# Kernel tuning notes

Hardware: AMD Instinct MI355X
Metric: run time of the kernel (lower is better)

The kernel has to match this reference:

```python
import jax, jax.numpy as jnp
import numpy as np

LN_EPS = 1e-5


def setup_inputs() -> dict:
    key = jax.random.key(0)
    ks = jax.random.split(key, 6)
    B, I, H = 16384, 512, 512
    x = jax.random.normal(ks[0], (B, I), dtype=jnp.float32)
    h_prev = jax.random.normal(ks[1], (B, H), dtype=jnp.float32)
    c_prev = jax.random.normal(ks[2], (B, H), dtype=jnp.float32)
    # packed gate weights in i|f|g|o order (equivalent to 8 separate matmuls)
    W_i = jax.random.normal(ks[3], (I, 4 * H), dtype=jnp.float32) * (1.0 / np.sqrt(I))
    W_h = jax.random.normal(ks[4], (H, 4 * H), dtype=jnp.float32) * (1.0 / np.sqrt(H))
    # biases: b_i=0, b_f=1, b_g=0, b_o=0 as in the torch module
    b = jnp.concatenate([jnp.zeros(H), jnp.ones(H), jnp.zeros(H), jnp.zeros(H)]).astype(jnp.float32)
    ln_weight = jnp.ones((H,), dtype=jnp.float32)
    ln_bias = jnp.zeros((H,), dtype=jnp.float32)
    return {"x": x, "h_prev": h_prev, "c_prev": c_prev, "W_i": W_i, "W_h": W_h,
            "b": b, "ln_weight": ln_weight, "ln_bias": ln_bias}


def layer_norm(h, w, bias):
    mu = jnp.mean(h, axis=-1, keepdims=True)
    var = jnp.var(h, axis=-1, keepdims=True)
    return (h - mu) * jax.lax.rsqrt(var + LN_EPS) * w + bias


def reference(x, h_prev, c_prev, W_i, W_h, b, ln_weight, ln_bias):
    H = h_prev.shape[-1]
    # two fused GEMMs covering all 4 gates: [B, 4H]
    gates = x @ W_i + h_prev @ W_h + b
    i, f, g, o = jnp.split(gates, 4, axis=-1)
    i = jax.nn.sigmoid(i)
    f = jax.nn.sigmoid(f)
    g = jnp.tanh(g)
    o = jax.nn.sigmoid(o)
    c = f * c_prev + i * g
    h = o * jnp.tanh(c)
    h = layer_norm(h, ln_weight, ln_bias)
    return (h, c)
```

## Files before the change

### kernel.cpp

```cpp
#include <hip/hip_runtime.h>
#include <cstdint>
#include <cstddef>

typedef unsigned short ushort_t;
typedef __attribute__((ext_vector_type(8))) short bf16x8;
typedef __attribute__((ext_vector_type(4))) float f32x4;

#define MROWS 16384
#define KDIM  1024
#define NDIM  2048
#define HDIM  512

static __device__ __forceinline__ unsigned short f2bf(float f) {
    unsigned int u = __float_as_uint(f);
    u += 0x7fffu + ((u >> 16) & 1u);
    return (unsigned short)(u >> 16);
}

static __device__ __forceinline__ float sigmoid_f(float x) {
    return 1.0f / (1.0f + __expf(-x));
}
static __device__ __forceinline__ float tanh_f(float x) {
    float t = __expf(2.0f * x);
    return 1.0f - 2.0f / (t + 1.0f);
}

__global__ __launch_bounds__(256) void pack_ab(const float* __restrict__ x,
                                               const float* __restrict__ hp,
                                               const float* __restrict__ Wi,
                                               const float* __restrict__ Wh,
                                               ushort_t* __restrict__ A,
                                               ushort_t* __restrict__ Bt) {
    __shared__ ushort_t sm[64][72];
    const int tid = threadIdx.x;
    if (blockIdx.x < 8192) {
        int t = blockIdx.x * 256 + tid;
        int row = t >> 7;
        int kc = (t & 127) << 3;
        const float* src = (kc < 512) ? (x + (size_t)row * 512 + kc)
                                      : (hp + (size_t)row * 512 + (kc - 512));
        float4 v0 = ((const float4*)src)[0];
        float4 v1 = ((const float4*)src)[1];
        ushort_t o[8] __attribute__((aligned(16)));
        o[0] = f2bf(v0.x); o[1] = f2bf(v0.y); o[2] = f2bf(v0.z); o[3] = f2bf(v0.w);
        o[4] = f2bf(v1.x); o[5] = f2bf(v1.y); o[6] = f2bf(v1.z); o[7] = f2bf(v1.w);
        *((uint4*)(A + (size_t)row * KDIM + kc)) = *((const uint4*)o);
    } else {
        int b2 = blockIdx.x - 8192;
        int kt = b2 >> 5;
        int ct = b2 & 31;
        const float* W = (kt < 8) ? (Wi + (size_t)(kt * 64) * NDIM)
                                  : (Wh + (size_t)((kt - 8) * 64) * NDIM);
        int c0 = (tid & 15) * 4;
        int r0 = tid >> 4;
#pragma unroll
        for (int r = 0; r < 4; ++r) {
            int krow = r * 16 + r0;
            float4 v = *((const float4*)(W + (size_t)krow * NDIM + ct * 64 + c0));
            sm[krow][c0 + 0] = f2bf(v.x);
            sm[krow][c0 + 1] = f2bf(v.y);
            sm[krow][c0 + 2] = f2bf(v.z);
            sm[krow][c0 + 3] = f2bf(v.w);
        }
        __syncthreads();
        int g = (ct * 64) >> 9;
        int h0 = ct * 64 - g * 512;
#pragma unroll
        for (int q = tid; q < 512; q += 256) {
            int cc = q >> 3;
            int kc = (q & 7) * 8;
            ushort_t o[8] __attribute__((aligned(16)));
#pragma unroll
            for (int j = 0; j < 8; ++j) o[j] = sm[kc + j][cc];
            int np = 4 * (h0 + cc) + g;
            *((uint4*)(Bt + (size_t)np * KDIM + kt * 64 + kc)) = *((const uint4*)o);
        }
    }
}

__global__ __launch_bounds__(256, 4) void gemm_cell(const ushort_t* __restrict__ A,
                                                    const ushort_t* __restrict__ Bt,
                                                    const float* __restrict__ b,
                                                    const float* __restrict__ c_prev,
                                                    float* __restrict__ h_out,
                                                    float* __restrict__ c_out) {
    __shared__ float smem_f[10240];
    ushort_t* Als = (ushort_t*)smem_f;
    ushort_t* Bls = Als + 256 * 64;

    const int tid  = threadIdx.x;
    const int w    = tid >> 6;
    const int lane = tid & 63;
    int bid = blockIdx.x;
    int lid = (bid >> 3) + (bid & 7) * 256;
    const int m0 = (lid >> 5) * 256;
    const int n0 = (lid & 31) * 64;
    const int wm = w * 64;
    const int lr   = lane & 15;
    const int quad = lane >> 4;
    const int sw   = lr & 7;

    f32x4 zero = {0.f, 0.f, 0.f, 0.f};
    f32x4 acc[4][4];
#pragma unroll
    for (int i = 0; i < 4; ++i)
#pragma unroll
        for (int j = 0; j < 4; ++j) acc[i][j] = zero;

    for (int kt = 0; kt < KDIM / 64; ++kt) {
#pragma unroll
        for (int r = 0; r < 8; ++r) {
            int c = r * 256 + tid;
            int trow = c >> 3;
            int chg = (c & 7) ^ (trow & 7);
            const ushort_t* ga = A + (size_t)(m0 + trow) * KDIM + kt * 64 + chg * 8;
            __builtin_amdgcn_global_load_lds(
                (const __attribute__((address_space(1))) void*)ga,
                (__attribute__((address_space(3))) void*)((char*)Als + c * 16),
                16, 0, 0);
        }
#pragma unroll
        for (int r = 0; r < 2; ++r) {
            int c = r * 256 + tid;
            int trow = c >> 3;
            int chg = (c & 7) ^ (trow & 7);
            const ushort_t* gb = Bt + (size_t)(n0 + trow) * KDIM + kt * 64 + chg * 8;
            __builtin_amdgcn_global_load_lds(
                (const __attribute__((address_space(1))) void*)gb,
                (__attribute__((address_space(3))) void*)((char*)Bls + c * 16),
                16, 0, 0);
        }
        __syncthreads();

#pragma unroll
        for (int kk = 0; kk < 2; ++kk) {
            bf16x8 af[4], bfr[4];
            int ch = kk * 4 + quad;
#pragma unroll
            for (int t2 = 0; t2 < 4; ++t2) {
                int ra = wm + t2 * 16 + lr;
                af[t2] = *((const bf16x8*)(Als + (ra * 8 + (ch ^ sw)) * 8));
            }
#pragma unroll
            for (int t2 = 0; t2 < 4; ++t2) {
                int rb = t2 * 16 + lr;
                bfr[t2] = *((const bf16x8*)(Bls + (rb * 8 + (ch ^ sw)) * 8));
            }
#pragma unroll
            for (int tm = 0; tm < 4; ++tm)
#pragma unroll
                for (int tn = 0; tn < 4; ++tn)
                    acc[tm][tn] = __builtin_amdgcn_mfma_f32_16x16x32_bf16(
                        af[tm], bfr[tn], acc[tm][tn], 0, 0, 0);
        }
        __syncthreads();
    }

    float* scr = smem_f + w * 1024;
    const int rr = lane >> 2;
    const int hg0 = (n0 >> 2) + (lane & 3) * 4;
    const float4 bi4 = *((const float4*)(b + hg0));
    const float4 bff = *((const float4*)(b + 512 + hg0));
    const float4 bgg = *((const float4*)(b + 1024 + hg0));
    const float4 boo = *((const float4*)(b + 1536 + hg0));
    const float bi[4] = {bi4.x, bi4.y, bi4.z, bi4.w};
    const float bfv[4] = {bff.x, bff.y, bff.z, bff.w};
    const float bg[4] = {bgg.x, bgg.y, bgg.z, bgg.w};
    const float bo[4] = {boo.x, boo.y, boo.z, boo.w};

#pragma unroll
    for (int tm = 0; tm < 4; ++tm) {
#pragma unroll
        for (int tn = 0; tn < 4; ++tn) {
            int c = tn * 16 + lr;
#pragma unroll
            for (int rg = 0; rg < 4; ++rg) {
                int r = quad * 4 + rg;
                int blk = (c >> 2) ^ r;
                scr[r * 64 + blk * 4 + (c & 3)] = acc[tm][tn][rg];
            }
        }
        float4 gv[4];
#pragma unroll
        for (int j = 0; j < 4; ++j) {
            int cb = (lane & 3) * 4 + j;
            gv[j] = *((const float4*)(scr + rr * 64 + (cb ^ rr) * 4));
        }
        int grow = m0 + wm + tm * 16 + rr;
        float4 cp4 = *((const float4*)(c_prev + (size_t)grow * HDIM + hg0));
        const float cpv[4] = {cp4.x, cp4.y, cp4.z, cp4.w};
        float cn[4], hv[4];
#pragma unroll
        for (int j = 0; j < 4; ++j) {
            float iv = sigmoid_f(gv[j].x + bi[j]);
            float fv = sigmoid_f(gv[j].y + bfv[j]);
            float g2 = tanh_f(gv[j].z + bg[j]);
            float ov = sigmoid_f(gv[j].w + bo[j]);
            cn[j] = fv * cpv[j] + iv * g2;
            hv[j] = ov * tanh_f(cn[j]);
        }
        float4 cno = {cn[0], cn[1], cn[2], cn[3]};
        float4 hvo = {hv[0], hv[1], hv[2], hv[3]};
        *((float4*)(c_out + (size_t)grow * HDIM + hg0)) = cno;
        *((float4*)(h_out + (size_t)grow * HDIM + hg0)) = hvo;
    }
}

__global__ __launch_bounds__(256) void ln_kernel(float* __restrict__ h,
                                                 const float* __restrict__ lw,
                                                 const float* __restrict__ lb) {
    int w = threadIdx.x >> 6;
    int lane = threadIdx.x & 63;
    int row = blockIdx.x * 4 + w;
    float* p = h + (size_t)row * HDIM + lane * 8;
    float4 a = ((const float4*)p)[0];
    float4 c = ((const float4*)p)[1];
    float s  = a.x + a.y + a.z + a.w + c.x + c.y + c.z + c.w;
    float ss = a.x * a.x + a.y * a.y + a.z * a.z + a.w * a.w +
               c.x * c.x + c.y * c.y + c.z * c.z + c.w * c.w;
#pragma unroll
    for (int off = 32; off > 0; off >>= 1) {
        s  += __shfl_xor(s, off);
        ss += __shfl_xor(ss, off);
    }
    float mu = s * (1.0f / 512.0f);
    float var = ss * (1.0f / 512.0f) - mu * mu;
    float rstd = rsqrtf(var + 1e-5f);
    const float* wp = lw + lane * 8;
    const float* bp = lb + lane * 8;
    float4 w0 = ((const float4*)wp)[0];
    float4 w1 = ((const float4*)wp)[1];
    float4 b0 = ((const float4*)bp)[0];
    float4 b1 = ((const float4*)bp)[1];
    a.x = (a.x - mu) * rstd * w0.x + b0.x;
    a.y = (a.y - mu) * rstd * w0.y + b0.y;
    a.z = (a.z - mu) * rstd * w0.z + b0.z;
    a.w = (a.w - mu) * rstd * w0.w + b0.w;
    c.x = (c.x - mu) * rstd * w1.x + b1.x;
    c.y = (c.y - mu) * rstd * w1.y + b1.y;
    c.z = (c.z - mu) * rstd * w1.z + b1.z;
    c.w = (c.w - mu) * rstd * w1.w + b1.w;
    ((float4*)p)[0] = a;
    ((float4*)p)[1] = c;
}

extern "C" void kernel_launch(void* const* d_in, const int* in_sizes, int n_in,
                              void* d_out, int out_size, void* d_ws, size_t ws_size,
                              hipStream_t stream) {
    const float* x      = (const float*)d_in[0];
    const float* h_prev = (const float*)d_in[1];
    const float* c_prev = (const float*)d_in[2];
    const float* W_i    = (const float*)d_in[3];
    const float* W_h    = (const float*)d_in[4];
    const float* b      = (const float*)d_in[5];
    const float* ln_w   = (const float*)d_in[6];
    const float* ln_b   = (const float*)d_in[7];

    float* h_out = (float*)d_out;
    float* c_out = h_out + (size_t)MROWS * HDIM;

    ushort_t* A  = (ushort_t*)d_ws;
    ushort_t* Bt = A + (size_t)MROWS * KDIM;

    pack_ab<<<8192 + 512, 256, 0, stream>>>(x, h_prev, W_i, W_h, A, Bt);
    gemm_cell<<<2048, 256, 0, stream>>>(A, Bt, b, c_prev, h_out, c_out);
    ln_kernel<<<MROWS / 4, 256, 0, stream>>>(h_out, ln_w, ln_b);
}
```

Measured before the change: 251.9 us.

## Enlarge GEMM tile to 256x256 with double-buffered LDS and prioritized MFMA phases

The GEMM block tile grows from 256x64 to 256x256, served by 512 threads as 8 waves in a 2x4 grid, each wave holding a 128x64 accumulator tile. Global-to-LDS loads are double-buffered two k-tiles ahead with explicit vmcnt waits, and compute is split into barrier-separated phases with s_setprio raised around the MFMA bursts. The larger tile raises operand reuse and the prefetch hides load latency. In exchange, register pressure and LDS use go up (128KB, capping occupancy) and the grid shrinks to 512 blocks.

New measurement: 247.3 us. No clear change (-1.8%).

```diff
diff --git a/kernel.cpp b/kernel.cpp
--- a/kernel.cpp
+++ b/kernel.cpp
@@ -10,6 +10,7 @@
 #define KDIM  1024
 #define NDIM  2048
 #define HDIM  512
+#define NTILE 16
 
 static __device__ __forceinline__ unsigned short f2bf(float f) {
     unsigned int u = __float_as_uint(f);
@@ -78,87 +79,154 @@
     }
 }
 
-__global__ __launch_bounds__(256, 4) void gemm_cell(const ushort_t* __restrict__ A,
+__global__ __launch_bounds__(512, 2) void gemm_cell(const ushort_t* __restrict__ A,
                                                     const ushort_t* __restrict__ Bt,
                                                     const float* __restrict__ b,
                                                     const float* __restrict__ c_prev,
                                                     float* __restrict__ h_out,
                                                     float* __restrict__ c_out) {
-    __shared__ float smem_f[10240];
-    ushort_t* Als = (ushort_t*)smem_f;
-    ushort_t* Bls = Als + 256 * 64;
+    __shared__ ushort_t lds[2][32768];
 
     const int tid  = threadIdx.x;
     const int w    = tid >> 6;
     const int lane = tid & 63;
+    const int mi   = w >> 2;
+    const int nj   = w & 3;
     int bid = blockIdx.x;
-    int lid = (bid >> 3) + (bid & 7) * 256;
-    const int m0 = (lid >> 5) * 256;
-    const int n0 = (lid & 31) * 64;
-    const int wm = w * 64;
+    int lid = (bid & 7) * 64 + (bid >> 3);
+    const int m0 = (lid >> 3) * 256;
+    const int n0 = (lid & 7) * 256;
     const int lr   = lane & 15;
     const int quad = lane >> 4;
     const int sw   = lr & 7;
 
-    f32x4 zero = {0.f, 0.f, 0.f, 0.f};
-    f32x4 acc[4][4];
-#pragma unroll
-    for (int i = 0; i < 4; ++i)
-#pragma unroll
-        for (int j = 0; j < 4; ++j) acc[i][j] = zero;
-
-    for (int kt = 0; kt < KDIM / 64; ++kt) {
-#pragma unroll
-        for (int r = 0; r < 8; ++r) {
-            int c = r * 256 + tid;
-            int trow = c >> 3;
-            int chg = (c & 7) ^ (trow & 7);
-            const ushort_t* ga = A + (size_t)(m0 + trow) * KDIM + kt * 64 + chg * 8;
-            __builtin_amdgcn_global_load_lds(
-                (const __attribute__((address_space(1))) void*)ga,
-                (__attribute__((address_space(3))) void*)((char*)Als + c * 16),
-                16, 0, 0);
-        }
-#pragma unroll
-        for (int r = 0; r < 2; ++r) {
-            int c = r * 256 + tid;
-            int trow = c >> 3;
-            int chg = (c & 7) ^ (trow & 7);
-            const ushort_t* gb = Bt + (size_t)(n0 + trow) * KDIM + kt * 64 + chg * 8;
-            __builtin_amdgcn_global_load_lds(
-                (const __attribute__((address_space(1))) void*)gb,
-                (__attribute__((address_space(3))) void*)((char*)Bls + c * 16),
-                16, 0, 0);
-        }
-        __syncthreads();
-
-#pragma unroll
-        for (int kk = 0; kk < 2; ++kk) {
-            bf16x8 af[4], bfr[4];
-            int ch = kk * 4 + quad;
-#pragma unroll
-            for (int t2 = 0; t2 < 4; ++t2) {
-                int ra = wm + t2 * 16 + lr;
-                af[t2] = *((const bf16x8*)(Als + (ra * 8 + (ch ^ sw)) * 8));
-            }
-#pragma unroll
-            for (int t2 = 0; t2 < 4; ++t2) {
-                int rb = t2 * 16 + lr;
-                bfr[t2] = *((const bf16x8*)(Bls + (rb * 8 + (ch ^ sw)) * 8));
-            }
-#pragma unroll
-            for (int tm = 0; tm < 4; ++tm)
-#pragma unroll
-                for (int tn = 0; tn < 4; ++tn)
-                    acc[tm][tn] = __builtin_amdgcn_mfma_f32_16x16x32_bf16(
-                        af[tm], bfr[tn], acc[tm][tn], 0, 0, 0);
-        }
-        __syncthreads();
+    const int trow0 = tid >> 3;
+    const int chg   = (tid & 7) ^ (trow0 & 7);
+    const size_t a_base = (size_t)(m0 + trow0) * KDIM + chg * 8;
+    const size_t b_base = (size_t)(n0 + trow0) * KDIM + chg * 8;
+    const int    l_base = tid * 16;
+
+#define STAGE(kt, bufi) do {                                                        \
+    const ushort_t* ap_ = A + a_base + (size_t)(kt) * 64;                           \
+    const ushort_t* bp_ = Bt + b_base + (size_t)(kt) * 64;                          \
+    char* al_ = (char*)&lds[bufi][0];                                               \
+    char* bl_ = (char*)&lds[bufi][16384];                                           \
+    _Pragma("unroll")                                                               \
+    for (int r_ = 0; r_ < 4; ++r_)                                                  \
+        __builtin_amdgcn_global_load_lds(                                           \
+            (const __attribute__((address_space(1))) void*)(ap_ + (size_t)r_ * 64 * KDIM), \
+            (__attribute__((address_space(3))) void*)(al_ + l_base + r_ * 8192),    \
+            16, 0, 0);                                                              \
+    _Pragma("unroll")                                                               \
+    for (int r_ = 0; r_ < 4; ++r_)                                                  \
+        __builtin_amdgcn_global_load_lds(                                           \
+            (const __attribute__((address_space(1))) void*)(bp_ + (size_t)r_ * 64 * KDIM), \
+            (__attribute__((address_space(3))) void*)(bl_ + l_base + r_ * 8192),    \
+            16, 0, 0);                                                              \
+} while (0)
+
+    f32x4 acc[8][4];
+#pragma unroll
+    for (int i = 0; i < 8; ++i)
+#pragma unroll
+        for (int j = 0; j < 4; ++j) acc[i][j] = (f32x4){0.f, 0.f, 0.f, 0.f};
+
+    STAGE(0, 0);
+    STAGE(1, 1);
+    asm volatile("s_waitcnt vmcnt(8)\n\ts_barrier" ::: "memory");
+
+#pragma unroll 2
+    for (int t = 0; t < NTILE; ++t) {
+        const ushort_t* Ab = &lds[t & 1][0];
+        const ushort_t* Bb = &lds[t & 1][16384];
+        bf16x8 af[4], bfr[4];
+
+#pragma unroll
+        for (int t2 = 0; t2 < 4; ++t2) {
+            int ra = mi * 128 + t2 * 16 + lr;
+            af[t2] = *((const bf16x8*)(Ab + (ra * 8 + (quad ^ sw)) * 8));
+        }
+#pragma unroll
+        for (int t3 = 0; t3 < 4; ++t3) {
+            int rb = nj * 64 + t3 * 16 + lr;
+            bfr[t3] = *((const bf16x8*)(Bb + (rb * 8 + (quad ^ sw)) * 8));
+        }
+        __builtin_amdgcn_s_barrier();
+        __builtin_amdgcn_s_setprio(1);
+#pragma unroll
+        for (int tm = 0; tm < 4; ++tm)
+#pragma unroll
+            for (int tn = 0; tn < 4; ++tn)
+                acc[tm][tn] = __builtin_amdgcn_mfma_f32_16x16x32_bf16(
+                    af[tm], bfr[tn], acc[tm][tn], 0, 0, 0);
+        __builtin_amdgcn_s_setprio(0);
+        __builtin_amdgcn_s_barrier();
+
+#pragma unroll
+        for (int t2 = 0; t2 < 4; ++t2) {
+            int ra = mi * 128 + (t2 + 4) * 16 + lr;
+            af[t2] = *((const bf16x8*)(Ab + (ra * 8 + (quad ^ sw)) * 8));
+        }
+        __builtin_amdgcn_s_barrier();
+        __builtin_amdgcn_s_setprio(1);
+#pragma unroll
+        for (int tm = 0; tm < 4; ++tm)
+#pragma unroll
+            for (int tn = 0; tn < 4; ++tn)
+                acc[tm + 4][tn] = __builtin_amdgcn_mfma_f32_16x16x32_bf16(
+                    af[tm], bfr[tn], acc[tm + 4][tn], 0, 0, 0);
+        __builtin_amdgcn_s_setprio(0);
+        __builtin_amdgcn_s_barrier();
+
+#pragma unroll
+        for (int t2 = 0; t2 < 4; ++t2) {
+            int ra = mi * 128 + t2 * 16 + lr;
+            af[t2] = *((const bf16x8*)(Ab + (ra * 8 + ((4 + quad) ^ sw)) * 8));
+        }
+#pragma unroll
+        for (int t3 = 0; t3 < 4; ++t3) {
+            int rb = nj * 64 + t3 * 16 + lr;
+            bfr[t3] = *((const bf16x8*)(Bb + (rb * 8 + ((4 + quad) ^ sw)) * 8));
+        }
+        __builtin_amdgcn_s_barrier();
+        __builtin_amdgcn_s_setprio(1);
+#pragma unroll
+        for (int tm = 0; tm < 4; ++tm)
+#pragma unroll
+            for (int tn = 0; tn < 4; ++tn)
+                acc[tm][tn] = __builtin_amdgcn_mfma_f32_16x16x32_bf16(
+                    af[tm], bfr[tn], acc[tm][tn], 0, 0, 0);
+        __builtin_amdgcn_s_setprio(0);
+        __builtin_amdgcn_s_barrier();
+
+#pragma unroll
+        for (int t2 = 0; t2 < 4; ++t2) {
+            int ra = mi * 128 + (t2 + 4) * 16 + lr;
+            af[t2] = *((const bf16x8*)(Ab + (ra * 8 + ((4 + quad) ^ sw)) * 8));
+        }
+        __builtin_amdgcn_s_barrier();
+        __builtin_amdgcn_s_setprio(1);
+#pragma unroll
+        for (int tm = 0; tm < 4; ++tm)
+#pragma unroll
+            for (int tn = 0; tn < 4; ++tn)
+                acc[tm + 4][tn] = __builtin_amdgcn_mfma_f32_16x16x32_bf16(
+                    af[tm], bfr[tn], acc[tm + 4][tn], 0, 0, 0);
+        __builtin_amdgcn_s_setprio(0);
+        asm volatile("s_waitcnt lgkmcnt(0)\n\ts_barrier" ::: "memory");
+
+        if (t < NTILE - 2) {
+            STAGE(t + 2, t & 1);
+            asm volatile("s_waitcnt vmcnt(8)\n\ts_barrier" ::: "memory");
+        } else if (t == NTILE - 2) {
+            asm volatile("s_waitcnt vmcnt(0)\n\ts_barrier" ::: "memory");
+        }
     }
-
-    float* scr = smem_f + w * 1024;
+#undef STAGE
+
+    float* scr = (float*)&lds[0][0] + w * 1024;
     const int rr = lane >> 2;
-    const int hg0 = (n0 >> 2) + (lane & 3) * 4;
+    const int hg0 = ((n0 + nj * 64) >> 2) + (lane & 3) * 4;
     const float4 bi4 = *((const float4*)(b + hg0));
     const float4 bff = *((const float4*)(b + 512 + hg0));
     const float4 bgg = *((const float4*)(b + 1024 + hg0));
@@ -169,7 +237,7 @@
     const float bo[4] = {boo.x, boo.y, boo.z, boo.w};
 
 #pragma unroll
-    for (int tm = 0; tm < 4; ++tm) {
+    for (int tm = 0; tm < 8; ++tm) {
 #pragma unroll
         for (int tn = 0; tn < 4; ++tn) {
             int c = tn * 16 + lr;
@@ -186,7 +254,7 @@
             int cb = (lane & 3) * 4 + j;
             gv[j] = *((const float4*)(scr + rr * 64 + (cb ^ rr) * 4));
         }
-        int grow = m0 + wm + tm * 16 + rr;
+        int grow = m0 + mi * 128 + tm * 16 + rr;
         float4 cp4 = *((const float4*)(c_prev + (size_t)grow * HDIM + hg0));
         const float cpv[4] = {cp4.x, cp4.y, cp4.z, cp4.w};
         float cn[4], hv[4];
@@ -263,6 +331,6 @@
     ushort_t* Bt = A + (size_t)MROWS * KDIM;
 
     pack_ab<<<8192 + 512, 256, 0, stream>>>(x, h_prev, W_i, W_h, A, Bt);
-    gemm_cell<<<2048, 256, 0, stream>>>(A, Bt, b, c_prev, h_out, c_out);
+    gemm_cell<<<512, 512, 0, stream>>>(A, Bt, b, c_prev, h_out, c_out);
     ln_kernel<<<MROWS / 4, 256, 0, stream>>>(h_out, ln_w, ln_b);
 }
```
